# Performance work log

Hardware: AMD Instinct MI355X
Metric: run time of the kernel (lower is better)

## Reference

```python
import jax, jax.numpy as jnp
import numpy as np

T_MAX = 0.3  # clamp ceiling for effective opacity (t_max init kwarg)


def setup_inputs() -> dict:
    key = jax.random.key(0)
    k0, k1, k2 = jax.random.split(key, 3)
    B, n_blobs, d_s, d_f = 1024, 131072, 64, 256
    return {
        "query": jax.random.normal(k0, (B, d_s), dtype=jnp.float32),
        "mu": jax.random.normal(k1, (n_blobs, d_s), dtype=jnp.float32) * 0.02,
        "log_var": jnp.zeros((n_blobs, d_s), dtype=jnp.float32),
        "raw_alpha": jnp.zeros((n_blobs,), dtype=jnp.float32),
        "features": jax.random.normal(k2, (n_blobs, d_f), dtype=jnp.float32) * 0.02,
        "log_tau": jnp.asarray(np.log(128.0), dtype=jnp.float32),
        "k": 16,
    }


def reference(query, mu, log_var, raw_alpha, features, log_tau, k):
    # query: [B, d_s]; mu/log_var: [N, d_s]; features: [N, d_f]
    tau = jnp.exp(log_tau)
    inv_var = jnp.exp(-log_var)                              # [N, d_s]
    # Mahalanobis distance expanded to avoid the [B, N, d_s] diff tensor:
    # sum_d (q - mu)^2 * iv = q^2.iv - 2 q.(mu*iv) + sum(mu^2*iv)
    q2 = jnp.einsum('bd,nd->bn', query * query, inv_var)      # [B, N]
    cross = jnp.einsum('bd,nd->bn', query, mu * inv_var)      # [B, N]
    m2 = jnp.sum(mu * mu * inv_var, axis=-1)                  # [N]
    mahal = q2 - 2.0 * cross + m2[None, :]
    K_all = jnp.exp(-0.5 * mahal / tau)                       # [B, N]
    alpha = jax.nn.sigmoid(raw_alpha)                         # [N]
    scores = K_all * alpha[None, :]
    top_scores, top_idx = jax.lax.top_k(scores, k)            # [B, k]

    # Gather selected blobs and recompute exact kernel (as in the original render)
    blob_feats = features[top_idx]                            # [B, k, d_f]
    blob_mu = mu[top_idx]                                     # [B, k, d_s]
    blob_iv = jnp.exp(-log_var[top_idx])                      # [B, k, d_s]
    diff = query[:, None, :] - blob_mu                        # [B, k, d_s]
    mahal_k = jnp.sum(diff * diff * blob_iv, axis=-1)         # [B, k]
    K_topk = jnp.exp(-0.5 * mahal_k / tau)
    blob_alpha = alpha[top_idx]                               # [B, k]

    # Alpha compositing in log space
    eff = jnp.minimum(blob_alpha * K_topk, T_MAX / k)         # [B, k]
    log_1m = jnp.log1p(-jnp.minimum(eff, 1.0 - 1e-6))
    log_cum = jnp.cumsum(log_1m, axis=-1)
    log_T = jnp.concatenate(
        [jnp.zeros_like(log_cum[:, :1]), log_cum[:, :-1]], axis=-1)
    weights = eff * jnp.exp(log_T)                            # [B, k]
    blob_meaning = jnp.einsum('bk,bkd->bd', weights, blob_feats)  # [B, d_f]
    t_residual = jnp.exp(log_cum[:, -1])                      # [B]
    return blob_meaning, t_residual
```

## Files before the change

### kernel.cpp

```cpp
#include <hip/hip_runtime.h>
#include <math.h>

#define BQ    1024
#define NB    131072
#define DS    64
#define DF    256
#define KSEL  16

#define QT    128
#define BC    64
#define PCH   64
#define NCHUNK (NB / BC)
#define CHUNKS_PER_BLK (NCHUNK/PCH)

#define CH_BYTES   32768
#define SPLIT_OFF  16384

typedef __bf16 bf16x8 __attribute__((ext_vector_type(8)));
typedef float  f32x4  __attribute__((ext_vector_type(4)));
typedef unsigned long long u64;

#define ENC_NEGINF 0x007FFFFFu

__device__ __forceinline__ unsigned map_f32(float s) {
    unsigned u = __float_as_uint(s);
    return (u & 0x80000000u) ? ~u : (u | 0x80000000u);
}

__device__ __forceinline__ float unmap_f32(unsigned e) {
    return __uint_as_float((e & 0x80000000u) ? (e & 0x7FFFFFFFu) : ~e);
}

__device__ __forceinline__ void async_cp16(const void* g, void* l) {
    __builtin_amdgcn_global_load_lds(
        (const __attribute__((address_space(1))) unsigned int*)g,
        (__attribute__((address_space(3))) unsigned int*)l, 16, 0, 0);
}

__global__ __launch_bounds__(256)
void prep_kernel(const float* __restrict__ mu,
                 const float* __restrict__ log_var,
                 const float* __restrict__ raw_alpha,
                 char* __restrict__ bprep,
                 float* __restrict__ m2la,
                 unsigned* __restrict__ gcut)
{
    int gid  = blockIdx.x * 256 + threadIdx.x;
    if (gid < BQ) gcut[gid] = ENC_NEGINF;
    int blob = gid >> 3;
    int dd   = gid & 7;

    const float* mrow = mu      + (size_t)blob * DS + dd * 8;
    const float* vrow = log_var + (size_t)blob * DS + dd * 8;
    float4 ma = ((const float4*)mrow)[0], mb = ((const float4*)mrow)[1];
    float4 va = ((const float4*)vrow)[0], vb = ((const float4*)vrow)[1];
    float m[8] = {ma.x, ma.y, ma.z, ma.w, mb.x, mb.y, mb.z, mb.w};
    float lv[8] = {va.x, va.y, va.z, va.w, vb.x, vb.y, vb.z, vb.w};

    bf16x8 hiv, liv, hmv, lmv;
    float p = 0.0f;
    #pragma unroll
    for (int j = 0; j < 8; ++j) {
        float iv = __expf(-lv[j]);
        float mv = m[j] * iv;
        p += m[j] * mv;
        __bf16 h1 = (__bf16)iv;  hiv[j] = h1; liv[j] = (__bf16)(iv - (float)h1);
        __bf16 h2 = (__bf16)mv;  hmv[j] = h2; lmv[j] = (__bf16)(mv - (float)h2);
    }
    p += __shfl_xor(p, 1);
    p += __shfl_xor(p, 2);
    p += __shfl_xor(p, 4);

    int c  = blob >> 6;
    int nt = (blob >> 4) & 3;
    int bl = blob & 15;
    int lane  = (dd & 3) * 16 + bl;
    int ks_iv = dd >> 2;
    int ks_mv = 2 + (dd >> 2);
    size_t b_iv = (size_t)c * CH_BYTES + nt * 4096 + ks_iv * 1024 + lane * 16;
    size_t b_mv = (size_t)c * CH_BYTES + nt * 4096 + ks_mv * 1024 + lane * 16;
    *(bf16x8*)(bprep + b_iv)             = hiv;
    *(bf16x8*)(bprep + b_iv + SPLIT_OFF) = liv;
    *(bf16x8*)(bprep + b_mv)             = hmv;
    *(bf16x8*)(bprep + b_mv + SPLIT_OFF) = lmv;

    if (dd == 0) {
        m2la[blob * 2]     = p;
        m2la[blob * 2 + 1] = -log1pf(__expf(-raw_alpha[blob]));
    }
}

__device__ __forceinline__ void ins16(float (&ts)[16], int (&ti)[16],
                                      float& mymin, float s, int idx)
{
    float v0[8]; int j0[8];
    #pragma unroll
    for (int i = 0; i < 8; ++i) {
        bool b = ts[2*i+1] < ts[2*i];
        v0[i] = b ? ts[2*i+1] : ts[2*i];
        j0[i] = (i << 1) | (b ? 1 : 0);
    }
    float v1[4]; int j1[4];
    #pragma unroll
    for (int i = 0; i < 4; ++i) {
        bool b = v0[2*i+1] < v0[2*i];
        v1[i] = b ? v0[2*i+1] : v0[2*i];
        j1[i] = b ? j0[2*i+1] : j0[2*i];
    }
    float v2[2]; int j2[2];
    #pragma unroll
    for (int i = 0; i < 2; ++i) {
        bool b = v1[2*i+1] < v1[2*i];
        v2[i] = b ? v1[2*i+1] : v1[2*i];
        j2[i] = b ? j1[2*i+1] : j1[2*i];
    }
    int am = (v2[1] < v2[0]) ? j2[1] : j2[0];
    #pragma unroll
    for (int i = 0; i < 16; ++i) {
        bool b = (i == am);
        ts[i] = b ? s : ts[i];
        ti[i] = b ? idx : ti[i];
    }
    float n0[8];
    #pragma unroll
    for (int i = 0; i < 8; ++i) n0[i] = fminf(ts[2*i], ts[2*i+1]);
    float n1[4];
    #pragma unroll
    for (int i = 0; i < 4; ++i) n1[i] = fminf(n0[2*i], n0[2*i+1]);
    mymin = fminf(fminf(n1[0], n1[1]), fminf(n1[2], n1[3]));
}

__device__ __forceinline__ float mux16(const f32x4 (&a)[4], int i)
{
    float v = a[0][0];
    v = (i == 1)  ? a[0][1] : v;  v = (i == 2)  ? a[0][2] : v;  v = (i == 3)  ? a[0][3] : v;
    v = (i == 4)  ? a[1][0] : v;  v = (i == 5)  ? a[1][1] : v;  v = (i == 6)  ? a[1][2] : v;
    v = (i == 7)  ? a[1][3] : v;  v = (i == 8)  ? a[2][0] : v;  v = (i == 9)  ? a[2][1] : v;
    v = (i == 10) ? a[2][2] : v;  v = (i == 11) ? a[2][3] : v;  v = (i == 12) ? a[3][0] : v;
    v = (i == 13) ? a[3][1] : v;  v = (i == 14) ? a[3][2] : v;  v = (i == 15) ? a[3][3] : v;
    return v;
}

__device__ __forceinline__ u64 shflxor64(u64 m, int mask)
{
    unsigned hi = __shfl_xor((unsigned)(m >> 32), mask);
    unsigned lo = __shfl_xor((unsigned)(m & 0xFFFFFFFFu), mask);
    return ((u64)hi << 32) | lo;
}

__global__ __launch_bounds__(256, 2)
void score_topk_kernel(const float* __restrict__ query,
                       const char* __restrict__ bprep,
                       const float* __restrict__ m2la,
                       const float* __restrict__ log_tau_p,
                       u64* __restrict__ cand,
                       unsigned* __restrict__ gcut)
{
    __shared__ __align__(16) short Bs[CH_BYTES / 2];

    const int tid   = threadIdx.x;
    const int lane  = tid & 63;
    const int quad  = lane >> 4;
    const int mrow  = lane & 15;
    const int wv    = tid >> 6;
    const int qbase = blockIdx.y * QT;

    const float nhit = -0.5f * expf(-log_tau_p[0]);

    bf16x8 ahi[2][4], alo[2][4];
    #pragma unroll
    for (int mt = 0; mt < 2; ++mt) {
        const float* qrow = query + (size_t)(qbase + wv * 32 + mt * 16 + mrow) * DS;
        #pragma unroll
        for (int ks = 0; ks < 4; ++ks) {
            int kq = ks * 32 + quad * 8;
            int d0 = kq & 63;
            bool lin = kq >= 64;
            bf16x8 h, l;
            #pragma unroll
            for (int j = 0; j < 8; ++j) {
                float v = qrow[d0 + j];
                float x = lin ? (-2.0f * v) : (v * v);
                __bf16 hb = (__bf16)x;
                h[j] = hb;
                l[j] = (__bf16)(x - (float)hb);
            }
            ahi[mt][ks] = h; alo[mt][ks] = l;
        }
    }

    float ts0[16], ts1[16]; int ti0[16], ti1[16];
    #pragma unroll
    for (int i = 0; i < 16; ++i) {
        ts0[i] = -INFINITY; ti0[i] = 0;
        ts1[i] = -INFINITY; ti1[i] = 0;
    }
    float my0 = -INFINITY, my1 = -INFINITY;
    unsigned* const gs0 = gcut + qbase + wv * 32 + mrow;
    unsigned* const gs1 = gcut + qbase + wv * 32 + 16 + mrow;

    const char* BsB = (const char*)Bs;

    int c = blockIdx.x;
    {
        const char* src = bprep + (size_t)c * CH_BYTES;
        #pragma unroll
        for (int i = 0; i < 8; ++i) {
            int s = tid + i * 256;
            async_cp16(src + s * 16, (void*)(BsB + s * 16));
        }
    }
    __syncthreads();

    for (int it = 0; it < CHUNKS_PER_BLK; ++it) {
        const int nbase = c * BC;
        const int cn    = c + PCH;
        const bool more = (it + 1) < CHUNKS_PER_BLK;

        float p0 = my0;
        p0 = fmaxf(p0, __shfl_xor(p0, 16)); p0 = fmaxf(p0, __shfl_xor(p0, 32));
        float p1 = my1;
        p1 = fmaxf(p1, __shfl_xor(p1, 16)); p1 = fmaxf(p1, __shfl_xor(p1, 32));
        unsigned e0 = ENC_NEGINF, e1 = ENC_NEGINF;
        if (quad == 0) e0 = atomicMax(gs0, map_f32(p0));
        if (quad == 1) e1 = atomicMax(gs1, map_f32(p1));

        float4 mlA[4], mlB[4];
        #pragma unroll
        for (int nt = 0; nt < 4; ++nt) {
            const float4* mp = (const float4*)&m2la[(size_t)(nbase + nt * 16 + quad * 4) * 2];
            mlA[nt] = mp[0]; mlB[nt] = mp[1];
        }

        f32x4 acc[2][4];
        #pragma unroll
        for (int nt = 0; nt < 4; ++nt) {
            bf16x8 bh[4], bl[4];
            #pragma unroll
            for (int ks = 0; ks < 4; ++ks) {
                bh[ks] = *(const bf16x8*)(BsB + nt * 4096 + ks * 1024 + lane * 16);
                bl[ks] = *(const bf16x8*)(BsB + SPLIT_OFF + nt * 4096 + ks * 1024 + lane * 16);
            }
            #pragma unroll
            for (int mt = 0; mt < 2; ++mt) {
                f32x4 a = {0.0f, 0.0f, 0.0f, 0.0f};
                #pragma unroll
                for (int ks = 0; ks < 4; ++ks) {
                    a = __builtin_amdgcn_mfma_f32_16x16x32_bf16(bh[ks], ahi[mt][ks], a, 0, 0, 0);
                    a = __builtin_amdgcn_mfma_f32_16x16x32_bf16(bl[ks], ahi[mt][ks], a, 0, 0, 0);
                    a = __builtin_amdgcn_mfma_f32_16x16x32_bf16(bh[ks], alo[mt][ks], a, 0, 0, 0);
                }
                acc[mt][nt] = a;
            }
        }
        __syncthreads();

        if (more) {
            const char* src = bprep + (size_t)cn * CH_BYTES;
            #pragma unroll
            for (int i = 0; i < 8; ++i) {
                int s = tid + i * 256;
                async_cp16(src + s * 16, (void*)(BsB + s * 16));
            }
        }

        unsigned ee0 = __shfl(e0, mrow);
        unsigned ee1 = __shfl(e1, 16 + mrow);
        const float gc0 = fmaxf(unmap_f32(ee0), p0);
        const float gc1 = fmaxf(unmap_f32(ee1), p1);

        {
            float cut = fmaxf(my0, gc0);
            unsigned gm = 0u;
            #pragma unroll
            for (int nt = 0; nt < 4; ++nt) {
                float m2_0 = mlA[nt].x, la_0 = mlA[nt].y;
                float m2_1 = mlA[nt].z, la_1 = mlA[nt].w;
                float m2_2 = mlB[nt].x, la_2 = mlB[nt].y;
                float m2_3 = mlB[nt].z, la_3 = mlB[nt].w;
                float s0 = nhit * (acc[0][nt][0] + m2_0) + la_0;
                float s1 = nhit * (acc[0][nt][1] + m2_1) + la_1;
                float s2 = nhit * (acc[0][nt][2] + m2_2) + la_2;
                float s3 = nhit * (acc[0][nt][3] + m2_3) + la_3;
                acc[0][nt][0] = s0; acc[0][nt][1] = s1;
                acc[0][nt][2] = s2; acc[0][nt][3] = s3;
                if (s0 > cut) gm |= 1u << (nt * 4);
                if (s1 > cut) gm |= 1u << (nt * 4 + 1);
                if (s2 > cut) gm |= 1u << (nt * 4 + 2);
                if (s3 > cut) gm |= 1u << (nt * 4 + 3);
            }
            while (__any(gm != 0u)) {
                if (gm) {
                    int i = __ffs(gm) - 1; gm &= gm - 1u;
                    float s = mux16(acc[0], i);
                    if (s > cut) {
                        ins16(ts0, ti0, my0, s, nbase + (i >> 2) * 16 + quad * 4 + (i & 3));
                        cut = fmaxf(my0, gc0);
                    }
                }
            }
        }
        {
            float cut = fmaxf(my1, gc1);
            unsigned gm = 0u;
            #pragma unroll
            for (int nt = 0; nt < 4; ++nt) {
                float m2_0 = mlA[nt].x, la_0 = mlA[nt].y;
                float m2_1 = mlA[nt].z, la_1 = mlA[nt].w;
                float m2_2 = mlB[nt].x, la_2 = mlB[nt].y;
                float m2_3 = mlB[nt].z, la_3 = mlB[nt].w;
                float s0 = nhit * (acc[1][nt][0] + m2_0) + la_0;
                float s1 = nhit * (acc[1][nt][1] + m2_1) + la_1;
                float s2 = nhit * (acc[1][nt][2] + m2_2) + la_2;
                float s3 = nhit * (acc[1][nt][3] + m2_3) + la_3;
                acc[1][nt][0] = s0; acc[1][nt][1] = s1;
                acc[1][nt][2] = s2; acc[1][nt][3] = s3;
                if (s0 > cut) gm |= 1u << (nt * 4);
                if (s1 > cut) gm |= 1u << (nt * 4 + 1);
                if (s2 > cut) gm |= 1u << (nt * 4 + 2);
                if (s3 > cut) gm |= 1u << (nt * 4 + 3);
            }
            while (__any(gm != 0u)) {
                if (gm) {
                    int i = __ffs(gm) - 1; gm &= gm - 1u;
                    float s = mux16(acc[1], i);
                    if (s > cut) {
                        ins16(ts1, ti1, my1, s, nbase + (i >> 2) * 16 + quad * 4 + (i & 3));
                        cut = fmaxf(my1, gc1);
                    }
                }
            }
        }

        __syncthreads();
        c = cn;
    }

    #pragma unroll
    for (int mt = 0; mt < 2; ++mt) {
        u64 k[16];
        #pragma unroll
        for (int i = 0; i < 16; ++i) {
            float  tsv = (mt == 0) ? ts0[i] : ts1[i];
            int    tiv = (mt == 0) ? ti0[i] : ti1[i];
            k[i] = ((u64)map_f32(tsv) << 32) | (u64)(0xFFFFFFFFu - (unsigned)tiv);
        }
        u64 outv[4];
        #pragma unroll
        for (int r = 0; r < 16; ++r) {
            u64 m = k[0];
            #pragma unroll
            for (int j = 1; j < 16; ++j) if (k[j] > m) m = k[j];
            u64 o = shflxor64(m, 16); if (o > m) m = o;
            o = shflxor64(m, 32);     if (o > m) m = o;
            #pragma unroll
            for (int j = 0; j < 16; ++j) if (k[j] == m) k[j] = 0ull;
            if ((r & 3) == quad) outv[r >> 2] = m;
        }
        u64* dst = cand + ((size_t)blockIdx.x * BQ + qbase + wv * 32 + mt * 16 + mrow) * KSEL;
        #pragma unroll
        for (int j = 0; j < 4; ++j)
            dst[quad + 4 * j] = outv[j];
    }
}

__global__ __launch_bounds__(256)
void merge_composite_kernel(const float* __restrict__ query,
                            const float* __restrict__ mu,
                            const float* __restrict__ log_var,
                            const float* __restrict__ raw_alpha,
                            const float* __restrict__ features,
                            const float* __restrict__ log_tau_p,
                            const u64* __restrict__ cand,
                            float* __restrict__ out)
{
    const int q   = blockIdx.x;
    const int tid = threadIdx.x;
    const int wv = tid >> 6, lane = tid & 63;

    __shared__ u64   wtop[4 * KSEL];
    __shared__ int   sel[KSEL];
    __shared__ float w_sh[KSEL];
    __shared__ float mah[KSEL];
    __shared__ float alp[KSEL];

    u64 k[4];
    #pragma unroll
    for (int r = 0; r < 4; ++r) {
        int g = wv * 256 + r * 64 + lane;
        k[r] = cand[((size_t)(g >> 4) * BQ + q) * KSEL + (g & 15)];
    }

    for (int r = 0; r < KSEL; ++r) {
        u64 m = k[0];
        #pragma unroll
        for (int j = 1; j < 4; ++j) if (k[j] > m) m = k[j];
        #pragma unroll
        for (int off = 32; off > 0; off >>= 1) {
            unsigned hi = __shfl_xor((unsigned)(m >> 32), off);
            unsigned lo = __shfl_xor((unsigned)(m & 0xFFFFFFFFu), off);
            u64 o = ((u64)hi << 32) | lo;
            if (o > m) m = o;
        }
        if (lane == 0) wtop[wv * KSEL + r] = m;
        #pragma unroll
        for (int j = 0; j < 4; ++j) if (k[j] == m) k[j] = 0ull;
    }
    __syncthreads();

    if (wv == 0) {
        u64 kk = wtop[lane];
        for (int r = 0; r < KSEL; ++r) {
            u64 m = kk;
            #pragma unroll
            for (int off = 32; off > 0; off >>= 1) {
                unsigned hi = __shfl_xor((unsigned)(m >> 32), off);
                unsigned lo = __shfl_xor((unsigned)(m & 0xFFFFFFFFu), off);
                u64 o = ((u64)hi << 32) | lo;
                if (o > m) m = o;
            }
            if (kk == m) kk = 0ull;
            if (lane == 0)
                sel[r] = (int)(0xFFFFFFFFu - (unsigned)(m & 0xFFFFFFFFull));
        }
    }
    __syncthreads();

    for (int r = wv; r < KSEL; r += 4) {
        int bi = sel[r];
        float qd = query[(size_t)q * DS + lane];
        float mv = mu[(size_t)bi * DS + lane];
        float d  = qd - mv;
        float t  = d * d * expf(-log_var[(size_t)bi * DS + lane]);
        #pragma unroll
        for (int off = 32; off > 0; off >>= 1) t += __shfl_down(t, off);
        if (lane == 0) {
            mah[r] = t;
            alp[r] = 1.0f / (1.0f + expf(-raw_alpha[bi]));
        }
    }
    __syncthreads();

    if (tid == 0) {
        float tau = expf(log_tau_p[0]);
        float cap = 0.3f / 16.0f;
        float logT = 0.0f;
        for (int r = 0; r < KSEL; ++r) {
            float K   = expf(-0.5f * mah[r] / tau);
            float eff = fminf(alp[r] * K, cap);
            w_sh[r]   = eff * expf(logT);
            logT     += log1pf(-fminf(eff, 1.0f - 1e-6f));
        }
        out[(size_t)BQ * DF + q] = expf(logT);
    }
    __syncthreads();

    {
        float a = 0.0f;
        #pragma unroll
        for (int r = 0; r < KSEL; ++r)
            a += w_sh[r] * features[(size_t)sel[r] * DF + tid];
        out[(size_t)q * DF + tid] = a;
    }
}

extern "C" void kernel_launch(void* const* d_in, const int* in_sizes, int n_in,
                              void* d_out, int out_size, void* d_ws, size_t ws_size,
                              hipStream_t stream)
{
    (void)in_sizes; (void)n_in; (void)out_size; (void)ws_size;
    const float* query     = (const float*)d_in[0];
    const float* mu        = (const float*)d_in[1];
    const float* log_var   = (const float*)d_in[2];
    const float* raw_alpha = (const float*)d_in[3];
    const float* features  = (const float*)d_in[4];
    const float* log_tau   = (const float*)d_in[5];
    float* out = (float*)d_out;

    char*  bprep = (char*)d_ws;
    float* m2la  = (float*)((char*)d_ws + (size_t)NCHUNK * CH_BYTES);
    u64*   cand  = (u64*)((char*)d_ws + (size_t)NCHUNK * CH_BYTES + (size_t)NB * 2 * 4);
    unsigned* gcut = (unsigned*)(out + (size_t)BQ * DF);

    prep_kernel<<<(NB * 8) / 256, 256, 0, stream>>>(mu, log_var, raw_alpha, bprep, m2la, gcut);

    dim3 g2(PCH, BQ / QT);
    score_topk_kernel<<<g2, 256, 0, stream>>>(query, bprep, m2la, log_tau, cand, gcut);

    merge_composite_kernel<<<BQ, 256, 0, stream>>>(query, mu, log_var, raw_alpha,
                                                   features, log_tau, cand, out);
}
```

Before: 622.2 us.

## Fold log-alpha into per-blob bias and threshold in unscaled distance space

The prep kernel folds the log-sigmoid alpha term into the m2 bias (scaled by -2*tau), which halves the per-blob side array read in the score loop. The score loop then compares raw accumulator sums against a threshold converted back from score space, with a small relative margin, and only scales by nhit for candidates that pass. The first chunk fills the top-16 lists directly instead of going through the insertion path. This trims per-element FMAs and loads in the hot filtering loop, at the cost of slightly different rounding that the margin is meant to absorb.

```diff
diff --git a/kernel.cpp b/kernel.cpp
--- a/kernel.cpp
+++ b/kernel.cpp
@@ -41,8 +41,9 @@
 void prep_kernel(const float* __restrict__ mu,
                  const float* __restrict__ log_var,
                  const float* __restrict__ raw_alpha,
+                 const float* __restrict__ log_tau_p,
                  char* __restrict__ bprep,
-                 float* __restrict__ m2la,
+                 float* __restrict__ m2a,
                  unsigned* __restrict__ gcut)
 {
     int gid  = blockIdx.x * 256 + threadIdx.x;
@@ -85,8 +86,9 @@
     *(bf16x8*)(bprep + b_mv + SPLIT_OFF) = lmv;
 
     if (dd == 0) {
-        m2la[blob * 2]     = p;
-        m2la[blob * 2 + 1] = -log1pf(__expf(-raw_alpha[blob]));
+        float la = -log1pf(__expf(-raw_alpha[blob]));
+        float inv_nhit = -2.0f * __expf(log_tau_p[0]);
+        m2a[blob] = p + la * inv_nhit;
     }
 }
 
@@ -151,7 +153,7 @@
 __global__ __launch_bounds__(256, 2)
 void score_topk_kernel(const float* __restrict__ query,
                        const char* __restrict__ bprep,
-                       const float* __restrict__ m2la,
+                       const float* __restrict__ m2a,
                        const float* __restrict__ log_tau_p,
                        u64* __restrict__ cand,
                        unsigned* __restrict__ gcut)
@@ -165,7 +167,8 @@
     const int wv    = tid >> 6;
     const int qbase = blockIdx.y * QT;
 
-    const float nhit = -0.5f * expf(-log_tau_p[0]);
+    const float nhit     = -0.5f * expf(-log_tau_p[0]);
+    const float inv_nhit = 1.0f / nhit;
 
     bf16x8 ahi[2][4], alo[2][4];
     #pragma unroll
@@ -225,12 +228,10 @@
         if (quad == 0) e0 = atomicMax(gs0, map_f32(p0));
         if (quad == 1) e1 = atomicMax(gs1, map_f32(p1));
 
-        float4 mlA[4], mlB[4];
-        #pragma unroll
-        for (int nt = 0; nt < 4; ++nt) {
-            const float4* mp = (const float4*)&m2la[(size_t)(nbase + nt * 16 + quad * 4) * 2];
-            mlA[nt] = mp[0]; mlB[nt] = mp[1];
-        }
+        f32x4 aA[4];
+        #pragma unroll
+        for (int nt = 0; nt < 4; ++nt)
+            aA[nt] = *(const f32x4*)&m2a[(size_t)(nbase + nt * 16 + quad * 4)];
 
         f32x4 acc[2][4];
         #pragma unroll
@@ -264,69 +265,92 @@
             }
         }
 
-        unsigned ee0 = __shfl(e0, mrow);
-        unsigned ee1 = __shfl(e1, 16 + mrow);
-        const float gc0 = fmaxf(unmap_f32(ee0), p0);
-        const float gc1 = fmaxf(unmap_f32(ee1), p1);
-
-        {
-            float cut = fmaxf(my0, gc0);
-            unsigned gm = 0u;
-            #pragma unroll
-            for (int nt = 0; nt < 4; ++nt) {
-                float m2_0 = mlA[nt].x, la_0 = mlA[nt].y;
-                float m2_1 = mlA[nt].z, la_1 = mlA[nt].w;
-                float m2_2 = mlB[nt].x, la_2 = mlB[nt].y;
-                float m2_3 = mlB[nt].z, la_3 = mlB[nt].w;
-                float s0 = nhit * (acc[0][nt][0] + m2_0) + la_0;
-                float s1 = nhit * (acc[0][nt][1] + m2_1) + la_1;
-                float s2 = nhit * (acc[0][nt][2] + m2_2) + la_2;
-                float s3 = nhit * (acc[0][nt][3] + m2_3) + la_3;
-                acc[0][nt][0] = s0; acc[0][nt][1] = s1;
-                acc[0][nt][2] = s2; acc[0][nt][3] = s3;
-                if (s0 > cut) gm |= 1u << (nt * 4);
-                if (s1 > cut) gm |= 1u << (nt * 4 + 1);
-                if (s2 > cut) gm |= 1u << (nt * 4 + 2);
-                if (s3 > cut) gm |= 1u << (nt * 4 + 3);
-            }
-            while (__any(gm != 0u)) {
-                if (gm) {
-                    int i = __ffs(gm) - 1; gm &= gm - 1u;
-                    float s = mux16(acc[0], i);
-                    if (s > cut) {
-                        ins16(ts0, ti0, my0, s, nbase + (i >> 2) * 16 + quad * 4 + (i & 3));
-                        cut = fmaxf(my0, gc0);
+        if (it == 0) {
+            #pragma unroll
+            for (int nt = 0; nt < 4; ++nt)
+                #pragma unroll
+                for (int reg = 0; reg < 4; ++reg) {
+                    int idx = nbase + nt * 16 + quad * 4 + reg;
+                    float s0 = nhit * (acc[0][nt][reg] + aA[nt][reg]);
+                    float s1 = nhit * (acc[1][nt][reg] + aA[nt][reg]);
+                    ts0[nt * 4 + reg] = s0; ti0[nt * 4 + reg] = idx;
+                    ts1[nt * 4 + reg] = s1; ti1[nt * 4 + reg] = idx;
+                }
+            float n0[8], n1[8];
+            #pragma unroll
+            for (int i = 0; i < 8; ++i) {
+                n0[i] = fminf(ts0[2*i], ts0[2*i+1]);
+                n1[i] = fminf(ts1[2*i], ts1[2*i+1]);
+            }
+            my0 = fminf(fminf(fminf(n0[0], n0[1]), fminf(n0[2], n0[3])),
+                        fminf(fminf(n0[4], n0[5]), fminf(n0[6], n0[7])));
+            my1 = fminf(fminf(fminf(n1[0], n1[1]), fminf(n1[2], n1[3])),
+                        fminf(fminf(n1[4], n1[5]), fminf(n1[6], n1[7])));
+        } else {
+            unsigned ee0 = __shfl(e0, mrow);
+            unsigned ee1 = __shfl(e1, 16 + mrow);
+            const float gc0 = fmaxf(unmap_f32(ee0), p0);
+            const float gc1 = fmaxf(unmap_f32(ee1), p1);
+
+            {
+                float cut = fmaxf(my0, gc0);
+                float T = cut * inv_nhit;
+                T = T + fabsf(T) * 2e-7f;
+                unsigned gm = 0u;
+                #pragma unroll
+                for (int nt = 0; nt < 4; ++nt) {
+                    float u0 = acc[0][nt][0] + aA[nt][0];
+                    float u1 = acc[0][nt][1] + aA[nt][1];
+                    float u2 = acc[0][nt][2] + aA[nt][2];
+                    float u3 = acc[0][nt][3] + aA[nt][3];
+                    acc[0][nt][0] = u0; acc[0][nt][1] = u1;
+                    acc[0][nt][2] = u2; acc[0][nt][3] = u3;
+                    if (u0 < T) gm |= 1u << (nt * 4);
+                    if (u1 < T) gm |= 1u << (nt * 4 + 1);
+                    if (u2 < T) gm |= 1u << (nt * 4 + 2);
+                    if (u3 < T) gm |= 1u << (nt * 4 + 3);
+                }
+                while (__any(gm != 0u)) {
+                    if (gm) {
+                        int i = __ffs(gm) - 1; gm &= gm - 1u;
+                        float s = nhit * mux16(acc[0], i);
+                        if (s > cut) {
+                            ins16(ts0, ti0, my0, s, nbase + (i >> 2) * 16 + quad * 4 + (i & 3));
+                            cut = fmaxf(my0, gc0);
+                            T = cut * inv_nhit;
+                            T = T + fabsf(T) * 2e-7f;
+                        }
                     }
                 }
             }
-        }
-        {
-            float cut = fmaxf(my1, gc1);
-            unsigned gm = 0u;
-            #pragma unroll
-            for (int nt = 0; nt < 4; ++nt) {
-                float m2_0 = mlA[nt].x, la_0 = mlA[nt].y;
-                float m2_1 = mlA[nt].z, la_1 = mlA[nt].w;
-                float m2_2 = mlB[nt].x, la_2 = mlB[nt].y;
-                float m2_3 = mlB[nt].z, la_3 = mlB[nt].w;
-                float s0 = nhit * (acc[1][nt][0] + m2_0) + la_0;
-                float s1 = nhit * (acc[1][nt][1] + m2_1) + la_1;
-                float s2 = nhit * (acc[1][nt][2] + m2_2) + la_2;
-                float s3 = nhit * (acc[1][nt][3] + m2_3) + la_3;
-                acc[1][nt][0] = s0; acc[1][nt][1] = s1;
-                acc[1][nt][2] = s2; acc[1][nt][3] = s3;
-                if (s0 > cut) gm |= 1u << (nt * 4);
-                if (s1 > cut) gm |= 1u << (nt * 4 + 1);
-                if (s2 > cut) gm |= 1u << (nt * 4 + 2);
-                if (s3 > cut) gm |= 1u << (nt * 4 + 3);
-            }
-            while (__any(gm != 0u)) {
-                if (gm) {
-                    int i = __ffs(gm) - 1; gm &= gm - 1u;
-                    float s = mux16(acc[1], i);
-                    if (s > cut) {
-                        ins16(ts1, ti1, my1, s, nbase + (i >> 2) * 16 + quad * 4 + (i & 3));
-                        cut = fmaxf(my1, gc1);
+            {
+                float cut = fmaxf(my1, gc1);
+                float T = cut * inv_nhit;
+                T = T + fabsf(T) * 2e-7f;
+                unsigned gm = 0u;
+                #pragma unroll
+                for (int nt = 0; nt < 4; ++nt) {
+                    float u0 = acc[1][nt][0] + aA[nt][0];
+                    float u1 = acc[1][nt][1] + aA[nt][1];
+                    float u2 = acc[1][nt][2] + aA[nt][2];
+                    float u3 = acc[1][nt][3] + aA[nt][3];
+                    acc[1][nt][0] = u0; acc[1][nt][1] = u1;
+                    acc[1][nt][2] = u2; acc[1][nt][3] = u3;
+                    if (u0 < T) gm |= 1u << (nt * 4);
+                    if (u1 < T) gm |= 1u << (nt * 4 + 1);
+                    if (u2 < T) gm |= 1u << (nt * 4 + 2);
+                    if (u3 < T) gm |= 1u << (nt * 4 + 3);
+                }
+                while (__any(gm != 0u)) {
+                    if (gm) {
+                        int i = __ffs(gm) - 1; gm &= gm - 1u;
+                        float s = nhit * mux16(acc[1], i);
+                        if (s > cut) {
+                            ins16(ts1, ti1, my1, s, nbase + (i >> 2) * 16 + quad * 4 + (i & 3));
+                            cut = fmaxf(my1, gc1);
+                            T = cut * inv_nhit;
+                            T = T + fabsf(T) * 2e-7f;
+                        }
                     }
                 }
             }
@@ -478,14 +502,15 @@
     float* out = (float*)d_out;
 
     char*  bprep = (char*)d_ws;
-    float* m2la  = (float*)((char*)d_ws + (size_t)NCHUNK * CH_BYTES);
+    float* m2a   = (float*)((char*)d_ws + (size_t)NCHUNK * CH_BYTES);
     u64*   cand  = (u64*)((char*)d_ws + (size_t)NCHUNK * CH_BYTES + (size_t)NB * 2 * 4);
     unsigned* gcut = (unsigned*)(out + (size_t)BQ * DF);
 
-    prep_kernel<<<(NB * 8) / 256, 256, 0, stream>>>(mu, log_var, raw_alpha, bprep, m2la, gcut);
+    prep_kernel<<<(NB * 8) / 256, 256, 0, stream>>>(mu, log_var, raw_alpha, log_tau,
+                                                    bprep, m2a, gcut);
 
     dim3 g2(PCH, BQ / QT);
-    score_topk_kernel<<<g2, 256, 0, stream>>>(query, bprep, m2la, log_tau, cand, gcut);
+    score_topk_kernel<<<g2, 256, 0, stream>>>(query, bprep, m2a, log_tau, cand, gcut);
 
     merge_composite_kernel<<<BQ, 256, 0, stream>>>(query, mu, log_var, raw_alpha,
                                                    features, log_tau, cand, out);
```

Result: faster. 557.7 us (-10.4%).
